# Kernel tuning notes

Hardware: AMD Instinct MI355X
Metric: run time of the kernel (lower is better)

## Reference

```python
import jax, jax.numpy as jnp
import numpy as np

DIM = 1536
NH = 12
HD = 128
EPS = 1e-6


def _rope(x, freqs, f, h, w, start):
    # x: [B,S,N,D] with S == f*h*w; freqs: [1024, D//2, 2] (real, imag) unit rotations
    B, S, N, D = x.shape
    c = D // 2
    c0 = c - 2 * (c // 3)
    c1 = c // 3
    ff = jnp.broadcast_to(freqs[start:start + f, :c0][:, None, None], (f, h, w, c0, 2))
    fh = jnp.broadcast_to(freqs[:h, c0:c0 + c1][None, :, None], (f, h, w, c1, 2))
    fw = jnp.broadcast_to(freqs[:w, c0 + c1:c][None, None, :], (f, h, w, c1, 2))
    fr = jnp.concatenate([ff, fh, fw], axis=3).reshape(S, 1, c, 2)  # [S,1,c,2]
    xr, xi = x[..., 0::2], x[..., 1::2]          # interleaved real/imag pairs
    cr, ci = fr[None, ..., 0], fr[None, ..., 1]  # [1,S,1,c]
    yr = xr * cr - xi * ci
    yi = xr * ci + xi * cr
    return jnp.stack([yr, yi], axis=-1).reshape(B, S, N, D)


def _rms(x, g):
    return x * jax.lax.rsqrt(jnp.mean(x * x, axis=-1, keepdims=True) + EPS) * g


def setup_inputs():
    key = jax.random.key(0)
    ks = jax.random.split(key, 16)
    S = 3 * 30 * 52  # chunk_size = 3 frames * 1560 tokens/frame
    x = jax.random.normal(ks[0], (1, S, DIM), jnp.float32)
    fr = jax.random.normal(ks[1], (1024, HD // 2, 2), jnp.float32)
    fr = fr / jnp.sqrt(jnp.sum(fr * fr, axis=-1, keepdims=True) + 1e-12)  # unit-modulus rotations
    g_kmean = jax.random.uniform(ks[2], (1, NH, HD), jnp.float32)  # mean of relu(k): nonnegative
    g_kv = jax.random.normal(ks[3], (1, NH, HD, HD), jnp.float32) * 0.05
    p = lambda i, shp: jax.random.normal(ks[i], shp, jnp.float32) * 0.02
    return dict(
        x=x, freqs=fr, g_kmean=g_kmean, g_kv=g_kv,
        Wq=p(4, (DIM, DIM)), bq=p(5, (DIM,)),
        Wk=p(6, (DIM, DIM)), bk=p(7, (DIM,)),
        Wv=p(8, (DIM, DIM)), bv=p(9, (DIM,)),
        Wo=p(10, (DIM, DIM)), bo=p(11, (DIM,)),
        gq=jnp.ones((DIM,), jnp.float32), gk=jnp.ones((DIM,), jnp.float32),
        Wlin=p(12, (HD, HD)), blin=p(13, (HD,)),
        f_frames=3, h_grid=30, w_grid=52,
    )


def reference(x, freqs, g_kmean, g_kv, Wq, bq, Wk, bk, Wv, bv, Wo, bo, gq, gk, Wlin, blin, f_frames, h_grid, w_grid):
    B, S, _ = x.shape
    q = _rms(x @ Wq.T + bq, gq).reshape(B, S, NH, HD)
    k = _rms(x @ Wk.T + bk, gk).reshape(B, S, NH, HD)
    v = (x @ Wv.T + bv).reshape(B, S, NH, HD)
    rq = _rope(q, freqs, f_frames, h_grid, w_grid, 0)
    rk = _rope(k, freqs, f_frames, h_grid, w_grid, 0)
    # local window attention: at step 0 (current_start=0, empty cache, sink_size=0)
    # the working kv window is exactly the roped current chunk
    scores = jnp.einsum('bsnd,btnd->bnst', rq, rk) * (HD ** -0.5)
    x_local = jnp.einsum('bnst,btnd->bsnd', jax.nn.softmax(scores, axis=-1), v)
    # global linear-attention branch (kernel_func = relu feature map on q, roped q against kv state)
    qf = jax.nn.relu(q)
    z = 1.0 / (jnp.einsum('bsnd,bnd->bsn', qf, g_kmean) + 1e-6)
    xg = jnp.einsum('bsnd,bndm->bsnm', rq, g_kv) * z[..., None]
    xg = xg @ Wlin.T + blin
    out = (x_local + xg).reshape(B, S, DIM) @ Wo.T + bo
    return out
```

## Files before the change

### kernel.cpp

```cpp
#include <hip/hip_runtime.h>

typedef short s16x8 __attribute__((ext_vector_type(8)));
typedef float f32x4 __attribute__((ext_vector_type(4)));
typedef float f32x16 __attribute__((ext_vector_type(16)));
typedef unsigned short u16x4 __attribute__((ext_vector_type(4)));
typedef unsigned int u32x4 __attribute__((ext_vector_type(4)));

#define QSCALE (0.08838834764831845f * 1.4426950408889634f)

__device__ __forceinline__ unsigned short f2bf(float f) {
  unsigned int u = __float_as_uint(f);
  u += 0x7fffu + ((u >> 16) & 1u);
  return (unsigned short)(u >> 16);
}
__device__ __forceinline__ float bf2f(unsigned short h) {
  return __uint_as_float((unsigned int)h << 16);
}
__device__ __forceinline__ float fast_exp2(float x) {
  float r;
  asm("v_exp_f32 %0, %1" : "=v"(r) : "v"(x));
  return r;
}

__device__ __forceinline__ void gload16(const void* gp, void* lp) {
  __builtin_amdgcn_global_load_lds(
      (const __attribute__((address_space(1))) void*)gp,
      (__attribute__((address_space(3))) void*)lp,
      16, 0, 0);
}

__global__ void cast_f32_bf16_x4(const float* __restrict__ in,
                                 unsigned short* __restrict__ out, int n4) {
  int i = blockIdx.x * 256 + threadIdx.x;
  if (i >= n4) return;
  f32x4 v = *((const f32x4*)in + i);
  u16x4 o;
  o[0] = f2bf(v[0]); o[1] = f2bf(v[1]); o[2] = f2bf(v[2]); o[3] = f2bf(v[3]);
  *((u16x4*)out + i) = o;
}

__global__ void cast_weights4(const float* __restrict__ Wq, const float* __restrict__ Wk,
                              const float* __restrict__ Wv, const float* __restrict__ Wo,
                              unsigned short* __restrict__ dst, int per4) {
  int i = blockIdx.x * 256 + threadIdx.x;
  if (i >= 4 * per4) return;
  int m = i / per4;
  int off = i - m * per4;
  const float* src = (m == 0) ? Wq : (m == 1) ? Wk : (m == 2) ? Wv : Wo;
  f32x4 v = *((const f32x4*)src + off);
  u16x4 o;
  o[0] = f2bf(v[0]); o[1] = f2bf(v[1]); o[2] = f2bf(v[2]); o[3] = f2bf(v[3]);
  *((u16x4*)dst + i) = o;
}

__global__ void g2fill_kernel(const float* __restrict__ g_kv,
                              const float* __restrict__ Wlin,
                              unsigned short* __restrict__ G2c) {
  int h = blockIdx.x, m = blockIdx.y, d = threadIdx.x;
  const float* gk = g_kv + ((size_t)h * 128 + d) * 128;
  const float* wl = Wlin + (size_t)m * 128;
  float s = 0.f;
  for (int j = 0; j < 128; ++j) s += gk[j] * wl[j];
  G2c[((size_t)h * 128 + m) * 128 + d] = f2bf(s * (1.0f / QSCALE));
}

template <int MODE, int NSPLIT>
__global__ __launch_bounds__(256) void gemm_bt(
    const unsigned short* __restrict__ A, const unsigned short* __restrict__ B,
    const float* __restrict__ bias, void* __restrict__ Cout,
    int M, int N, int K, int lda, int ldb,
    const float* __restrict__ o0buf, const float* __restrict__ zbuf,
    const float* __restrict__ o1buf, const float* __restrict__ lbuf) {
  __shared__ __align__(16) unsigned short Asm_[128 * 64];
  __shared__ __align__(16) unsigned short Bsm_[128 * 64];
  const int tid = threadIdx.x;
  const int wid = tid >> 6, lane = tid & 63;
  const int mt = blockIdx.x, nt = blockIdx.y;
  const int wr = wid >> 1, wc = wid & 1;
  const int acol = (MODE == 3) ? nt * 128 : 0;
  f32x4 acc[4][4] = {};

  const int st_srccol = ((((lane & 7) << 4) ^ ((lane >> 3) << 4)) >> 1);
  const int st_rowoff = (lane >> 3);

  for (int k0 = 0; k0 < K; k0 += 64) {
    __syncthreads();
#pragma unroll
    for (int r = 0; r < 4; ++r) {
      int c = wid * 4 + r;
      int lrow = c * 8 + st_rowoff;
      int arow = mt * 128 + lrow; if (arow > M - 1) arow = M - 1;
      gload16(A + (size_t)arow * lda + acol + k0 + st_srccol,
              (char*)Asm_ + c * 1024 + lane * 16);
      int brow = nt * 128 + lrow;
      gload16(B + (size_t)brow * ldb + k0 + st_srccol,
              (char*)Bsm_ + c * 1024 + lane * 16);
    }
    __syncthreads();
#pragma unroll
    for (int kk = 0; kk < 2; ++kk) {
      int cb = (kk * 64 + ((lane >> 4) << 4)) ^ ((lane & 7) << 4);
      s16x8 af[4], bfr[4];
#pragma unroll
      for (int m = 0; m < 4; ++m)
        af[m] = *(const s16x8*)((const char*)Asm_ + (wr * 64 + m * 16 + (lane & 15)) * 128 + cb);
#pragma unroll
      for (int n = 0; n < 4; ++n)
        bfr[n] = *(const s16x8*)((const char*)Bsm_ + (wc * 64 + n * 16 + (lane & 15)) * 128 + cb);
#pragma unroll
      for (int m = 0; m < 4; ++m)
#pragma unroll
        for (int n = 0; n < 4; ++n)
          acc[m][n] = __builtin_amdgcn_mfma_f32_16x16x32_bf16(af[m], bfr[n], acc[m][n], 0, 0, 0);
    }
  }
  const int rb = mt * 128 + wr * 64, cbse = nt * 128 + wc * 64;
#pragma unroll
  for (int m = 0; m < 4; ++m) {
#pragma unroll
    for (int n = 0; n < 4; ++n) {
#pragma unroll
      for (int rg = 0; rg < 4; ++rg) {
        int rr = rb + m * 16 + ((lane >> 4) << 2) + rg;
        int cc = cbse + n * 16 + (lane & 15);
        if (rr < M) {
          float v = acc[m][n][rg];
          if (MODE == 0) {
            v += bias[cc];
            ((unsigned short*)Cout)[(size_t)rr * N + cc] = f2bf(v);
          } else if (MODE == 1) {
            v += bias[cc];
            ((float*)Cout)[(size_t)rr * N + cc] = v;
          } else {
            int hd = cc >> 7;
            float lsum = lbuf[(size_t)rr * 12 + hd];
            float osum = o0buf[(size_t)rr * N + cc];
#pragma unroll
            for (int s = 1; s < NSPLIT; ++s) {
              lsum += lbuf[((size_t)s * M + rr) * 12 + hd];
              osum += o1buf[(size_t)(s - 1) * M * 1536 + (size_t)rr * N + cc];
            }
            v = v * zbuf[(size_t)rr * 12 + hd] + osum * (1.0f / lsum) + bias[cc & 127];
            ((unsigned short*)Cout)[(size_t)rr * N + cc] = f2bf(v);
          }
        }
      }
    }
  }
}

__global__ __launch_bounds__(256) void rms_rope_kernel(
    const unsigned short* __restrict__ qkv, const float* __restrict__ freqs,
    const float* __restrict__ gq, const float* __restrict__ gk,
    const float* __restrict__ g_kmean,
    unsigned short* __restrict__ rqb, unsigned short* __restrict__ rkb,
    float* __restrict__ zbuf, int S,
    const int* __restrict__ hgp, const int* __restrict__ wgp) {
  const int s = blockIdx.x;
  const int isk = blockIdx.y;
  const unsigned short* row = qkv + (size_t)s * 4608 + (isk ? 1536 : 0);
  const float* g = isk ? gk : gq;
  unsigned short* outr = isk ? rkb : rqb;
  float* zout = isk ? nullptr : zbuf;
  const float oscale = isk ? 1.0f : QSCALE;
  const int tid = threadIdx.x;
  const int lane = tid & 63, wid = tid >> 6;
  unsigned int pv0, pv1, pv2;
  float ssq = 0.f;
  {
    pv0 = *(const unsigned int*)(row + 2 * (tid));
    pv1 = *(const unsigned int*)(row + 2 * (tid + 256));
    pv2 = *(const unsigned int*)(row + 2 * (tid + 512));
    float a0 = bf2f((unsigned short)(pv0 & 0xffffu)), b0 = bf2f((unsigned short)(pv0 >> 16));
    float a1 = bf2f((unsigned short)(pv1 & 0xffffu)), b1 = bf2f((unsigned short)(pv1 >> 16));
    float a2 = bf2f((unsigned short)(pv2 & 0xffffu)), b2 = bf2f((unsigned short)(pv2 >> 16));
    ssq = a0 * a0 + b0 * b0 + a1 * a1 + b1 * b1 + a2 * a2 + b2 * b2;
  }
#pragma unroll
  for (int m = 1; m < 64; m <<= 1) ssq += __shfl_xor(ssq, m, 64);
  __shared__ float wpart[4];
  if (lane == 0) wpart[wid] = ssq;
  __syncthreads();
  float tot = wpart[0] + wpart[1] + wpart[2] + wpart[3];
  float rms = rsqrtf(tot * (1.0f / 1536.0f) + 1e-6f);
  const int Wg = *wgp;
  const int HWg = (*hgp) * Wg;
  int fi = s / HWg; int rem = s - fi * HWg;
  int hi = rem / Wg; int wi = rem - hi * Wg;
  unsigned int pvs[3] = {pv0, pv1, pv2};
#pragma unroll
  for (int rd = 0; rd < 3; ++rd) {
    int p = tid + rd * 256;
    int c = p & 63;
    int fidx = (c < 22) ? fi : ((c < 43) ? hi : wi);
    float cr = freqs[fidx * 128 + 2 * c];
    float ci = freqs[fidx * 128 + 2 * c + 1];
    float xr = bf2f((unsigned short)(pvs[rd] & 0xffffu)) * rms * g[2 * p];
    float xi = bf2f((unsigned short)(pvs[rd] >> 16)) * rms * g[2 * p + 1];
    float yr = (xr * cr - xi * ci) * oscale;
    float yi = (xr * ci + xi * cr) * oscale;
    unsigned int ow = (unsigned int)f2bf(yr) | ((unsigned int)f2bf(yi) << 16);
    *(unsigned int*)(outr + (size_t)s * 1536 + 2 * p) = ow;
    if (zout != nullptr) {
      int head = p >> 6;
      float part = fmaxf(xr, 0.f) * g_kmean[head * 128 + 2 * c] +
                   fmaxf(xi, 0.f) * g_kmean[head * 128 + 2 * c + 1];
#pragma unroll
      for (int m = 1; m < 64; m <<= 1) part += __shfl_xor(part, m, 64);
      if (lane == 0) zout[(size_t)s * 12 + head] = 1.0f / (part + 1e-6f);
    }
  }
}

__global__ __launch_bounds__(256) void vtrans_kernel(const unsigned short* __restrict__ vpre,
                                                     unsigned short* __restrict__ vt, int S, int ld) {
  __shared__ unsigned short tile[64][66];
  int t0 = blockIdx.x * 64, c0 = blockIdx.y * 64;
  int tid = threadIdx.x;
#pragma unroll
  for (int rep = 0; rep < 16; ++rep) {
    int lin = rep * 256 + tid;
    int i = lin >> 6, j = lin & 63;
    int t = t0 + i; if (t > S - 1) t = S - 1;
    tile[i][j] = vpre[(size_t)t * ld + c0 + j];
  }
  __syncthreads();
#pragma unroll
  for (int rep = 0; rep < 16; ++rep) {
    int lin = rep * 256 + tid;
    int j = lin >> 6, i = lin & 63;
    int t = t0 + i;
    if (t < S) vt[(size_t)(c0 + j) * S + t] = tile[i][j];
  }
}

__global__ __launch_bounds__(256, 3) void attn_kernel(
    const unsigned short* __restrict__ rq, const unsigned short* __restrict__ rk,
    const unsigned short* __restrict__ vt, float* __restrict__ o0buf,
    float* __restrict__ o1buf, float* __restrict__ lbuf, int S, int nqb, int nsplit) {
  __shared__ __align__(16) unsigned short Ks[2][32 * 128];
  __shared__ __align__(16) unsigned short Vs[2][32 * 128];
  const int tid = threadIdx.x, wid = tid >> 6, lane = tid & 63;
  const int q32 = lane & 31, hi = lane >> 5;

  const int total = nqb * 12 * nsplit;
  int lg = blockIdx.x;
  if ((total & 7) == 0) lg = (lg & 7) * (total >> 3) + (lg >> 3);
  const int z = lg / (nqb * 12);
  int rem = lg - z * nqb * 12;
  const int h = rem / nqb;
  const int qb = rem - h * nqb;
  const int q0 = qb * 128 + wid * 32;

  const int seg = (((S + nsplit - 1) / nsplit) + 31) & ~31;
  const int tbeg = z * seg;
  const int tend = (tbeg + seg < S) ? (tbeg + seg) : S;
  float* obufz = (z == 0) ? o0buf : (o1buf + (size_t)(z - 1) * S * 1536);
  float* lbufz = lbuf + (size_t)z * S * 12;

  s16x8 qf[8];
  {
    int qrow = q0 + q32; if (qrow > S - 1) qrow = S - 1;
    const unsigned short* qp = rq + (size_t)qrow * 1536 + h * 128 + hi * 8;
#pragma unroll
    for (int dblk = 0; dblk < 8; ++dblk) qf[dblk] = *(const s16x8*)(qp + dblk * 16);
  }
  f32x16 o0 = {}, o1 = {}, o2 = {}, o3 = {};
  float lsum = 0.f;

  const int st_row0 = tid >> 4;
  const int st_off = (tid & 15) * 16;
  const int kswz = (q32 & 15) << 4;
  const int vswz = (q32 & 15) << 4;

#define STAGE(buf, t0s)                                                            \
  {                                                                                \
    _Pragma("unroll") for (int r = 0; r < 2; ++r) {                                \
      int row = st_row0 + 16 * r;                                                  \
      int key = (row & 15) << 4;                                                   \
           \
      int kL = st_off ^ key;                                                       \
      int trow = (t0s) + row; if (trow > S - 1) trow = S - 1;                      \
      gload16(rk + (size_t)trow * 1536 + h * 128 + (kL >> 1),                      \
              (char*)Ks[buf] + r * 4096 + tid * 16);                               \
           \
      int vL = st_off ^ key;                                                       \
      int vd = row + 32 * (vL >> 6);                                               \
      int vtok = (t0s) + ((vL & 63) >> 1); if (vtok > S - 8) vtok = S - 8;         \
      gload16(vt + (size_t)(h * 128 + vd) * S + vtok,                              \
              (char*)Vs[buf] + r * 4096 + tid * 16);                               \
    }                                                                              \
  }

  STAGE(0, tbeg);
  __syncthreads();
  int cur = 0;
  for (int t0 = tbeg; t0 < tend; t0 += 32) {
    if (t0 + 32 < tend) STAGE(cur ^ 1, t0 + 32);
    f32x16 sc = {};
    __builtin_amdgcn_s_setprio(1);
#pragma unroll
    for (int dblk = 0; dblk < 8; ++dblk) {
      s16x8 kfr = *(const s16x8*)((const char*)Ks[cur] + q32 * 256 +
                                  ((dblk * 32 + hi * 16) ^ kswz));
      sc = __builtin_amdgcn_mfma_f32_32x32x16_bf16(kfr, qf[dblk], sc, 0, 0, 0);
    }
    __builtin_amdgcn_s_setprio(0);
    const bool full = (t0 + 32 <= tend);
    unsigned int pk[8];
    float rs = 0.f;
#pragma unroll
    for (int j = 0; j < 8; ++j) {
      float p0, p1;
      if (full) {
        p0 = fast_exp2(sc[2 * j]);
        p1 = fast_exp2(sc[2 * j + 1]);
      } else {
        int r0 = 2 * j;
        int tk0 = t0 + (r0 & 3) + 8 * (r0 >> 2) + 4 * hi;
        p0 = (tk0 < tend) ? fast_exp2(sc[2 * j]) : 0.f;
        p1 = (tk0 + 1 < tend) ? fast_exp2(sc[2 * j + 1]) : 0.f;
      }
      unsigned int u0 = __float_as_uint(p0) & 0xffff0000u;
      unsigned int u1 = __float_as_uint(p1) & 0xffff0000u;
      rs += __uint_as_float(u0) + __uint_as_float(u1);
      pk[j] = (u0 >> 16) | u1;
    }
    lsum += rs;
    unsigned int x0 = pk[0], y0 = pk[2], x1 = pk[1], y1 = pk[3];
    asm("v_permlane32_swap_b32 %0, %1" : "+v"(x0), "+v"(y0));
    asm("v_permlane32_swap_b32 %0, %1" : "+v"(x1), "+v"(y1));
    unsigned int x2 = pk[4], y2 = pk[6], x3 = pk[5], y3 = pk[7];
    asm("v_permlane32_swap_b32 %0, %1" : "+v"(x2), "+v"(y2));
    asm("v_permlane32_swap_b32 %0, %1" : "+v"(x3), "+v"(y3));
    u32x4 pa0v = {x0, x1, y0, y1};
    u32x4 pa1v = {x2, x3, y2, y3};
    s16x8 pa0 = __builtin_bit_cast(s16x8, pa0v);
    s16x8 pa1 = __builtin_bit_cast(s16x8, pa1v);
    __builtin_amdgcn_s_setprio(1);
    {
      const char* vrowb = (const char*)Vs[cur] + q32 * 256;
#pragma unroll
      for (int ks = 0; ks < 2; ++ks) {
        s16x8 pa = ks ? pa1 : pa0;
        s16x8 vb;
        vb = *(const s16x8*)(vrowb + ((0 * 64 + ks * 32 + hi * 16) ^ vswz));
        o0 = __builtin_amdgcn_mfma_f32_32x32x16_bf16(pa, vb, o0, 0, 0, 0);
        vb = *(const s16x8*)(vrowb + ((1 * 64 + ks * 32 + hi * 16) ^ vswz));
        o1 = __builtin_amdgcn_mfma_f32_32x32x16_bf16(pa, vb, o1, 0, 0, 0);
        vb = *(const s16x8*)(vrowb + ((2 * 64 + ks * 32 + hi * 16) ^ vswz));
        o2 = __builtin_amdgcn_mfma_f32_32x32x16_bf16(pa, vb, o2, 0, 0, 0);
        vb = *(const s16x8*)(vrowb + ((3 * 64 + ks * 32 + hi * 16) ^ vswz));
        o3 = __builtin_amdgcn_mfma_f32_32x32x16_bf16(pa, vb, o3, 0, 0, 0);
      }
    }
    __builtin_amdgcn_s_setprio(0);
    __syncthreads();
    cur ^= 1;
  }
  lsum += __shfl_xor(lsum, 32, 64);
  {
    int qrow = q0 + q32;
    if (hi == 0 && qrow < S) lbufz[(size_t)qrow * 12 + h] = lsum;
  }
#pragma unroll
  for (int r = 0; r < 16; ++r) {
    int qrow = q0 + (r & 3) + 8 * (r >> 2) + 4 * hi;
    if (qrow < S) {
      float* orow = obufz + (size_t)qrow * 1536 + h * 128 + q32;
      orow[0] = o0[r]; orow[32] = o1[r]; orow[64] = o2[r]; orow[96] = o3[r];
    }
  }
#undef STAGE
}

extern "C" void kernel_launch(void* const* d_in, const int* in_sizes, int n_in,
                              void* d_out, int out_size, void* d_ws, size_t ws_size,
                              hipStream_t stream) {
  const float* x = (const float*)d_in[0];
  const float* freqs = (const float*)d_in[1];
  const float* g_kmean = (const float*)d_in[2];
  const float* g_kv = (const float*)d_in[3];
  const float* Wq = (const float*)d_in[4];  const float* bq = (const float*)d_in[5];
  const float* Wk = (const float*)d_in[6];  const float* bk = (const float*)d_in[7];
  const float* Wv = (const float*)d_in[8];  const float* bv = (const float*)d_in[9];
  const float* Wo = (const float*)d_in[10]; const float* bo = (const float*)d_in[11];
  const float* gq = (const float*)d_in[12]; const float* gk = (const float*)d_in[13];
  const float* Wlin = (const float*)d_in[14]; const float* blin = (const float*)d_in[15];
  const int* hgp = (const int*)d_in[17];
  const int* wgp = (const int*)d_in[18];

  const int S = in_sizes[0] / 1536;

  char* ws = (char*)d_ws;
  const size_t SZ = (size_t)S * 1536 * 2;
  const size_t OSZ = (size_t)S * 1536 * 4;
  const size_t WSZ = (size_t)1536 * 1536 * 2;
  const size_t QKVSZ = (size_t)S * 4608 * 2;
  const size_t G2SZ = (size_t)12 * 128 * 128 * 2;
  size_t o_xbf = 0;
  size_t o_wqkv = o_xbf + SZ;
  size_t o_wo = o_wqkv + 3 * WSZ;
  size_t o_g2 = o_wo + WSZ;
  size_t o_qkv = o_g2 + G2SZ;
  size_t o_rk = o_qkv + QKVSZ;
  size_t o_vt = o_rk + SZ;
  size_t o_z = o_vt + SZ;
  size_t o_bqkv = o_z + (size_t)S * 12 * 4;
  size_t o_o1 = o_bqkv + 4608 * 4;

  int nsplit = 3;
  if (ws_size < o_o1 + (size_t)2 * OSZ + (size_t)3 * S * 12 * 4) nsplit = 2;
  size_t o_l = o_o1 + (size_t)(nsplit - 1) * OSZ;
  size_t need = o_l + (size_t)nsplit * S * 12 * 4;
  if (ws_size < need) return;

  unsigned short* xbf = (unsigned short*)(ws + o_xbf);
  unsigned short* wqkv = (unsigned short*)(ws + o_wqkv);
  unsigned short* wob = (unsigned short*)(ws + o_wo);
  unsigned short* g2c = (unsigned short*)(ws + o_g2);
  unsigned short* qkv = (unsigned short*)(ws + o_qkv);
  unsigned short* rkb = (unsigned short*)(ws + o_rk);
  unsigned short* vtb = (unsigned short*)(ws + o_vt);
  float* zbuf = (float*)(ws + o_z);
  float* bqkv = (float*)(ws + o_bqkv);
  unsigned short* rqb = xbf;
  float* o0buf = (float*)(ws + o_qkv);
  float* o1buf = (float*)(ws + o_o1);
  float* lbuf = (float*)(ws + o_l);
  unsigned short* ybf = (unsigned short*)(ws + o_qkv + OSZ);

  {
    int n4 = (S * 1536) / 4;
    cast_f32_bf16_x4<<<(n4 + 255) / 256, 256, 0, stream>>>(x, xbf, n4);
    int per4 = (1536 * 1536) / 4;
    cast_weights4<<<(4 * per4 + 255) / 256, 256, 0, stream>>>(Wq, Wk, Wv, Wo, wqkv, per4);
  }
  hipMemcpyAsync(bqkv, bq, 1536 * 4, hipMemcpyDeviceToDevice, stream);
  hipMemcpyAsync(bqkv + 1536, bk, 1536 * 4, hipMemcpyDeviceToDevice, stream);
  hipMemcpyAsync(bqkv + 3072, bv, 1536 * 4, hipMemcpyDeviceToDevice, stream);

  g2fill_kernel<<<dim3(12, 128), 128, 0, stream>>>(g_kv, Wlin, g2c);

  {
    dim3 ggrid((S + 127) / 128, 36);
    gemm_bt<0, 2><<<ggrid, 256, 0, stream>>>(xbf, wqkv, bqkv, qkv, S, 4608, 1536, 1536, 1536,
                                             nullptr, nullptr, nullptr, nullptr);
  }

  rms_rope_kernel<<<dim3(S, 2), 256, 0, stream>>>(qkv, freqs, gq, gk, g_kmean,
                                                  rqb, rkb, zbuf, S, hgp, wgp);

  vtrans_kernel<<<dim3((S + 63) / 64, 24), 256, 0, stream>>>(qkv + 3072, vtb, S, 4608);

  {
    int nqb = (S + 127) / 128;
    attn_kernel<<<dim3(nqb * 12 * nsplit), 256, 0, stream>>>(rqb, rkb, vtb,
                                                             o0buf, o1buf, lbuf, S, nqb, nsplit);
  }

  {
    dim3 ggrid((S + 127) / 128, 12);
    if (nsplit == 3) {
      gemm_bt<3, 3><<<ggrid, 256, 0, stream>>>(rqb, g2c, blin, ybf, S, 1536, 128, 1536, 128,
                                               o0buf, zbuf, o1buf, lbuf);
    } else {
      gemm_bt<3, 2><<<ggrid, 256, 0, stream>>>(rqb, g2c, blin, ybf, S, 1536, 128, 1536, 128,
                                               o0buf, zbuf, o1buf, lbuf);
    }
    gemm_bt<1, 2><<<ggrid, 256, 0, stream>>>(ybf, wob, bo, (float*)d_out, S, 1536, 1536, 1536, 1536,
                                             nullptr, nullptr, nullptr, nullptr);
  }
}
```

Before: 405.2 us.

## Store split-attention partial outputs in bf16 and add XCD-aware GEMM tile remap

Attention partial outputs (o0/o1 split buffers) are now written as bf16 instead of fp32, and the output-projection epilogue converts them back when combining splits. This halves the memory traffic for the split-K attention partials and shrinks the workspace. Separately, the GEMM kernel remaps its block index so that consecutive tiles land on the same XCD, which is meant to improve L2 reuse across the chiplets. Rounding the partial sums to bf16 before normalization adds some precision loss.

```diff
diff --git a/kernel.cpp b/kernel.cpp
--- a/kernel.cpp
+++ b/kernel.cpp
@@ -69,13 +69,18 @@
     const unsigned short* __restrict__ A, const unsigned short* __restrict__ B,
     const float* __restrict__ bias, void* __restrict__ Cout,
     int M, int N, int K, int lda, int ldb,
-    const float* __restrict__ o0buf, const float* __restrict__ zbuf,
-    const float* __restrict__ o1buf, const float* __restrict__ lbuf) {
+    const unsigned short* __restrict__ o0buf, const float* __restrict__ zbuf,
+    const unsigned short* __restrict__ o1buf, const float* __restrict__ lbuf) {
   __shared__ __align__(16) unsigned short Asm_[128 * 64];
   __shared__ __align__(16) unsigned short Bsm_[128 * 64];
   const int tid = threadIdx.x;
   const int wid = tid >> 6, lane = tid & 63;
-  const int mt = blockIdx.x, nt = blockIdx.y;
+  int nwg = gridDim.x * gridDim.y;
+  int gid = blockIdx.x + blockIdx.y * gridDim.x;
+  int q8 = nwg >> 3, r8 = nwg & 7;
+  int xcd = gid & 7, jj = gid >> 3;
+  int sw = (xcd < r8 ? xcd * (q8 + 1) : r8 * (q8 + 1) + (xcd - r8) * q8) + jj;
+  const int mt = sw % gridDim.x, nt = sw / gridDim.x;
   const int wr = wid >> 1, wc = wid & 1;
   const int acol = (MODE == 3) ? nt * 128 : 0;
   f32x4 acc[4][4] = {};
@@ -134,11 +139,11 @@
           } else {
             int hd = cc >> 7;
             float lsum = lbuf[(size_t)rr * 12 + hd];
-            float osum = o0buf[(size_t)rr * N + cc];
+            float osum = bf2f(o0buf[(size_t)rr * N + cc]);
 #pragma unroll
             for (int s = 1; s < NSPLIT; ++s) {
               lsum += lbuf[((size_t)s * M + rr) * 12 + hd];
-              osum += o1buf[(size_t)(s - 1) * M * 1536 + (size_t)rr * N + cc];
+              osum += bf2f(o1buf[(size_t)(s - 1) * M * 1536 + (size_t)rr * N + cc]);
             }
             v = v * zbuf[(size_t)rr * 12 + hd] + osum * (1.0f / lsum) + bias[cc & 127];
             ((unsigned short*)Cout)[(size_t)rr * N + cc] = f2bf(v);
@@ -236,8 +241,8 @@
 
 __global__ __launch_bounds__(256, 3) void attn_kernel(
     const unsigned short* __restrict__ rq, const unsigned short* __restrict__ rk,
-    const unsigned short* __restrict__ vt, float* __restrict__ o0buf,
-    float* __restrict__ o1buf, float* __restrict__ lbuf, int S, int nqb, int nsplit) {
+    const unsigned short* __restrict__ vt, unsigned short* __restrict__ o0buf,
+    unsigned short* __restrict__ o1buf, float* __restrict__ lbuf, int S, int nqb, int nsplit) {
   __shared__ __align__(16) unsigned short Ks[2][32 * 128];
   __shared__ __align__(16) unsigned short Vs[2][32 * 128];
   const int tid = threadIdx.x, wid = tid >> 6, lane = tid & 63;
@@ -255,7 +260,7 @@
   const int seg = (((S + nsplit - 1) / nsplit) + 31) & ~31;
   const int tbeg = z * seg;
   const int tend = (tbeg + seg < S) ? (tbeg + seg) : S;
-  float* obufz = (z == 0) ? o0buf : (o1buf + (size_t)(z - 1) * S * 1536);
+  unsigned short* obufz = (z == 0) ? o0buf : (o1buf + (size_t)(z - 1) * S * 1536);
   float* lbufz = lbuf + (size_t)z * S * 12;
 
   s16x8 qf[8];
@@ -278,12 +283,10 @@
     _Pragma("unroll") for (int r = 0; r < 2; ++r) {                                \
       int row = st_row0 + 16 * r;                                                  \
       int key = (row & 15) << 4;                                                   \
-           \
       int kL = st_off ^ key;                                                       \
       int trow = (t0s) + row; if (trow > S - 1) trow = S - 1;                      \
       gload16(rk + (size_t)trow * 1536 + h * 128 + (kL >> 1),                      \
               (char*)Ks[buf] + r * 4096 + tid * 16);                               \
-           \
       int vL = st_off ^ key;                                                       \
       int vd = row + 32 * (vL >> 6);                                               \
       int vtok = (t0s) + ((vL & 63) >> 1); if (vtok > S - 8) vtok = S - 8;         \
@@ -367,8 +370,9 @@
   for (int r = 0; r < 16; ++r) {
     int qrow = q0 + (r & 3) + 8 * (r >> 2) + 4 * hi;
     if (qrow < S) {
-      float* orow = obufz + (size_t)qrow * 1536 + h * 128 + q32;
-      orow[0] = o0[r]; orow[32] = o1[r]; orow[64] = o2[r]; orow[96] = o3[r];
+      unsigned short* orow = obufz + (size_t)qrow * 1536 + h * 128 + q32;
+      orow[0] = f2bf(o0[r]); orow[32] = f2bf(o1[r]);
+      orow[64] = f2bf(o2[r]); orow[96] = f2bf(o3[r]);
     }
   }
 #undef STAGE
@@ -394,7 +398,6 @@
 
   char* ws = (char*)d_ws;
   const size_t SZ = (size_t)S * 1536 * 2;
-  const size_t OSZ = (size_t)S * 1536 * 4;
   const size_t WSZ = (size_t)1536 * 1536 * 2;
   const size_t QKVSZ = (size_t)S * 4608 * 2;
   const size_t G2SZ = (size_t)12 * 128 * 128 * 2;
@@ -410,8 +413,8 @@
   size_t o_o1 = o_bqkv + 4608 * 4;
 
   int nsplit = 3;
-  if (ws_size < o_o1 + (size_t)2 * OSZ + (size_t)3 * S * 12 * 4) nsplit = 2;
-  size_t o_l = o_o1 + (size_t)(nsplit - 1) * OSZ;
+  if (ws_size < o_o1 + (size_t)2 * SZ + (size_t)3 * S * 12 * 4) nsplit = 2;
+  size_t o_l = o_o1 + (size_t)(nsplit - 1) * SZ;
   size_t need = o_l + (size_t)nsplit * S * 12 * 4;
   if (ws_size < need) return;
 
@@ -425,10 +428,10 @@
   float* zbuf = (float*)(ws + o_z);
   float* bqkv = (float*)(ws + o_bqkv);
   unsigned short* rqb = xbf;
-  float* o0buf = (float*)(ws + o_qkv);
-  float* o1buf = (float*)(ws + o_o1);
+  unsigned short* o0buf = (unsigned short*)(ws + o_qkv);
+  unsigned short* o1buf = (unsigned short*)(ws + o_o1);
   float* lbuf = (float*)(ws + o_l);
-  unsigned short* ybf = (unsigned short*)(ws + o_qkv + OSZ);
+  unsigned short* ybf = (unsigned short*)(ws + o_qkv + SZ);
 
   {
     int n4 = (S * 1536) / 4;
```

Measured after the change: 398.8 us. About the same (-1.6%).
